# Performance work log

Measured on AMD Instinct MI355X. Metric: run time of the kernel, lower is better.

The kernel has to match this reference:

```python
import jax, jax.numpy as jnp
import numpy as np

D_MODEL = 1024
D_FF = 4096
NUM_EXPERTS = 8
TOP_K = 2
TEMPERATURE = 1.0


def setup_inputs() -> dict:
    key = jax.random.key(0)
    ks = jax.random.split(key, 5)
    hidden_states = jax.random.normal(ks[0], (4, 2048, D_MODEL), dtype=jnp.float32)
    # Router gate: nn.Linear(d_model, num_experts, bias=False), weight [E, d], std=0.01
    gate_w = jax.random.normal(ks[1], (NUM_EXPERTS, D_MODEL), dtype=jnp.float32) * 0.01
    # Expert FFN weights: torch Linear weight is [out, in]; init std=0.02, biases zero
    w1 = jax.random.normal(ks[2], (NUM_EXPERTS, D_FF, D_MODEL), dtype=jnp.float32) * 0.02
    b1 = jnp.zeros((NUM_EXPERTS, D_FF), dtype=jnp.float32)
    w2 = jax.random.normal(ks[3], (NUM_EXPERTS, D_MODEL, D_FF), dtype=jnp.float32) * 0.02
    b2 = jnp.zeros((NUM_EXPERTS, D_MODEL), dtype=jnp.float32)
    return {"hidden_states": hidden_states, "gate_w": gate_w,
            "w1": w1, "b1": b1, "w2": w2, "b2": b2}


def reference(hidden_states, gate_w, w1, b1, w2, b2):
    B, S, D = hidden_states.shape
    E, K = NUM_EXPERTS, TOP_K
    x = hidden_states.reshape(-1, D)  # [T, d]
    T = x.shape[0]

    # --- Router (fp32, eval mode: no noise) ---
    logits = jnp.einsum('td,ed->te', x, gate_w) / TEMPERATURE  # [T, E]
    probs = jax.nn.softmax(logits, axis=-1)
    top_vals, top_idx = jax.lax.top_k(probs, K)               # [T, K]
    weights = top_vals / jnp.sum(top_vals, axis=-1, keepdims=True)

    # Dense combine weights per expert: [T, E]
    one_hot = jax.nn.one_hot(top_idx, E, dtype=x.dtype)        # [T, K, E]
    combine = jnp.einsum('tke,tk->te', one_hot, weights)       # [T, E]

    # --- Load-balancing aux loss ---
    importance = jnp.mean(probs, axis=0)                       # [E]
    load = jnp.sum(one_hot, axis=(0, 1)) / (T * K)             # [E]
    aux_loss = E * jnp.sum(importance * load)

    # --- Expert dispatch/combine (loop over fixed small E) ---
    out = jnp.zeros_like(x)
    for e in range(E):
        h = jax.nn.gelu(x @ w1[e].T + b1[e], approximate=False)  # [T, d_ff]
        y = h @ w2[e].T + b2[e]                                   # [T, d]
        out = out + combine[:, e:e + 1] * y

    return out.reshape(B, S, D), aux_loss
```

## Files before the change

### kernel.cpp

```cpp
#include <hip/hip_runtime.h>
#include <cstdint>
#include <math.h>

#define T_TOK 8192
#define DM 1024
#define DFF 4096
#define NE 8
#define WLMAX 136

typedef __attribute__((ext_vector_type(8))) short short8;
typedef __attribute__((ext_vector_type(4))) float f32x4;

#define GLDS16(g, l) __builtin_amdgcn_global_load_lds( \
    (const __attribute__((address_space(1))) void*)(g), \
    (__attribute__((address_space(3))) void*)(l), 16, 0, 0)

static __device__ __forceinline__ unsigned short f2bf(float f) {
    union { float f; unsigned int u; } v; v.f = f;
    unsigned int r = (v.u + 0x7FFFu + ((v.u >> 16) & 1u)) >> 16;
    return (unsigned short)r;
}

static __device__ __forceinline__ float gelu_f(float v) {
    float z = fabsf(v) * 0.70710678118654752f;
    float t = 1.f / (1.f + 0.3275911f * z);
    float p = t * (0.254829592f + t * (-0.284496736f + t * (1.421413741f +
              t * (-1.453152027f + t * 1.061405429f))));
    float erfz = 1.f - p * __expf(-z * z);
    float s = (v >= 0.f) ? erfz : -erfz;
    return 0.5f * v * (1.f + s);
}

__global__ __launch_bounds__(256) void conv_flat(const float* __restrict__ src,
                                                 unsigned short* __restrict__ dst,
                                                 long long n)
{
    long long i = ((long long)blockIdx.x * 256 + threadIdx.x) * 4;
    if (i >= n) return;
    const float4 v = *(const float4*)(src + i);
    uint2 u;
    u.x = (unsigned)f2bf(v.x) | ((unsigned)f2bf(v.y) << 16);
    u.y = (unsigned)f2bf(v.z) | ((unsigned)f2bf(v.w) << 16);
    *(uint2*)(dst + i) = u;
}

__global__ __launch_bounds__(256) void conv_rows(const float* __restrict__ src,
                                                 unsigned short* __restrict__ dst,
                                                 long long src_off, long long src_stride,
                                                 int ncols)
{
    long long row = blockIdx.y;
    int c = (blockIdx.x * 256 + threadIdx.x) * 4;
    if (c >= ncols) return;
    const float4 v = *(const float4*)(src + src_off + row * src_stride + c);
    uint2 u;
    u.x = (unsigned)f2bf(v.x) | ((unsigned)f2bf(v.y) << 16);
    u.y = (unsigned)f2bf(v.z) | ((unsigned)f2bf(v.w) << 16);
    *(uint2*)(dst + row * (long long)ncols + c) = u;
}

__global__ __launch_bounds__(256) void router_kernel(
    const float* __restrict__ x, const float* __restrict__ gw,
    int* __restrict__ counts, float* __restrict__ imp,
    int* __restrict__ ptok, float* __restrict__ pw)
{
    __shared__ float4 sgw[NE * 256];
    __shared__ float simp[NE];
    const int tid = threadIdx.x;
    #pragma unroll
    for (int j = 0; j < 8; ++j) sgw[tid + j * 256] = ((const float4*)gw)[tid + j * 256];
    if (tid < NE) simp[tid] = 0.f;
    __syncthreads();

    const int wid = tid >> 6, lane = tid & 63;
    const int t = blockIdx.x * 4 + wid;
    float acc[NE];
    #pragma unroll
    for (int e = 0; e < NE; ++e) acc[e] = 0.f;
    const float4* xr = (const float4*)(x + (size_t)t * DM);
    #pragma unroll
    for (int j = 0; j < 4; ++j) {
        int idx = lane + j * 64;
        float4 xv = xr[idx];
        #pragma unroll
        for (int e = 0; e < NE; ++e) {
            float4 g = sgw[e * 256 + idx];
            acc[e] += xv.x * g.x + xv.y * g.y + xv.z * g.z + xv.w * g.w;
        }
    }
    #pragma unroll
    for (int off = 32; off; off >>= 1) {
        #pragma unroll
        for (int e = 0; e < NE; ++e) acc[e] += __shfl_xor(acc[e], off);
    }
    if (lane == 0) {
        float m = acc[0];
        #pragma unroll
        for (int e = 1; e < NE; ++e) m = fmaxf(m, acc[e]);
        float p[NE], s = 0.f;
        #pragma unroll
        for (int e = 0; e < NE; ++e) { p[e] = expf(acc[e] - m); s += p[e]; }
        float inv = 1.f / s;
        #pragma unroll
        for (int e = 0; e < NE; ++e) { p[e] *= inv; atomicAdd(&simp[e], p[e]); }
        int i0 = 0;
        #pragma unroll
        for (int e = 1; e < NE; ++e) if (p[e] > p[i0]) i0 = e;
        int i1 = (i0 == 0) ? 1 : 0;
        #pragma unroll
        for (int e = 0; e < NE; ++e) if (e != i0 && p[e] > p[i1]) i1 = e;
        float v0 = p[i0], v1 = p[i1], wsum = v0 + v1;
        int s0 = atomicAdd(&counts[i0], 1);
        ptok[i0 * T_TOK + s0] = t; pw[i0 * T_TOK + s0] = v0 / wsum;
        int s1 = atomicAdd(&counts[i1], 1);
        ptok[i1 * T_TOK + s1] = t; pw[i1 * T_TOK + s1] = v1 / wsum;
    }
    __syncthreads();
    if (tid < NE) atomicAdd(&imp[tid], simp[tid]);
}

__global__ void finalize_kernel(const int* __restrict__ counts,
                                const float* __restrict__ imp,
                                int* __restrict__ offs, int* __restrict__ wl,
                                float* __restrict__ aux_out)
{
    if (threadIdx.x == 0 && blockIdx.x == 0) {
        int o = 0; float aux = 0.f;
        for (int e = 0; e < NE; ++e) {
            offs[e] = o; o += counts[e];
            aux += (imp[e] / (float)T_TOK) * ((float)counts[e] / (float)(T_TOK * 2));
        }
        offs[NE] = o;
        int it = 0;
        for (int e = 0; e < NE; ++e) {
            int mts = (counts[e] + 127) >> 7;
            for (int mt = 0; mt < mts; ++mt) wl[it++] = (e << 16) | mt;
        }
        for (; it < WLMAX; ++it) wl[it] = -1;
        *aux_out = (float)NE * aux;
    }
}

__global__ __launch_bounds__(256) void pregather_kernel(
    const float* __restrict__ x, const int* __restrict__ counts,
    const int* __restrict__ offs, const int* __restrict__ ptok,
    unsigned short* __restrict__ xg, int* __restrict__ tc, int* __restrict__ tokpair)
{
    const int e = blockIdx.y;
    const int slot = blockIdx.x * 4 + (threadIdx.x >> 6);
    if (slot >= counts[e]) return;
    const int tok = ptok[e * T_TOK + slot];
    const int lane = threadIdx.x & 63;
    const int p = offs[e] + slot;
    if (lane == 0) {
        int k = atomicAdd(&tc[tok], 1);
        tokpair[tok * 2 + k] = p;
    }
    const float4* src = (const float4*)(x + (size_t)tok * DM);
    uint2* dst = (uint2*)(xg + (size_t)p * DM);
    #pragma unroll
    for (int j = 0; j < 4; ++j) {
        float4 v = src[lane + j * 64];
        uint2 u;
        u.x = (unsigned)f2bf(v.x) | ((unsigned)f2bf(v.y) << 16);
        u.y = (unsigned)f2bf(v.z) | ((unsigned)f2bf(v.w) << 16);
        dst[lane + j * 64] = u;
    }
}

__global__ __launch_bounds__(256) void combine_kernel(
    const float* __restrict__ yv, const int* __restrict__ tokpair,
    float* __restrict__ out)
{
    const int t = blockIdx.x;
    const int c = threadIdx.x;
    const long long p0 = tokpair[t * 2], p1 = tokpair[t * 2 + 1];
    const float4 a = ((const float4*)(yv + p0 * DM))[c];
    const float4 b = ((const float4*)(yv + p1 * DM))[c];
    float4 o;
    o.x = a.x + b.x; o.y = a.y + b.y; o.z = a.z + b.z; o.w = a.w + b.w;
    ((float4*)(out + (long long)t * DM))[c] = o;
}

template<int EPI>
__global__ __launch_bounds__(256, 2) void gemm_bt(
    const unsigned short* __restrict__ A,
    const unsigned short* __restrict__ W,
    const float* __restrict__ bias,
    const int* __restrict__ counts, const int* __restrict__ offs,
    const int* __restrict__ ptok, const float* __restrict__ pw,
    const int* __restrict__ wl,
    unsigned short* __restrict__ Hout, float* __restrict__ yv,
    int FFC, int cch, int wfull)
{
    const int bx = blockIdx.x;
    const int item = wl[(bx & 7) * 17 + (bx >> 3)];
    if (item < 0) return;
    const int e = item >> 16, mt = item & 0xffff;
    const int n_e = counts[e];
    int rows_here = n_e - mt * 128; if (rows_here > 128) rows_here = 128;
    const long long row_lo = (long long)offs[e] + (long long)mt * 128;
    const int nt = blockIdx.y;
    const int KD = (EPI == 0) ? DM : FFC;

    __shared__ unsigned short lA[128 * 64];
    __shared__ unsigned short lB[256 * 64];

    const int tid = threadIdx.x, lane = tid & 63, wid = tid >> 6;
    const int nsub = wid * 64;
    const int hi = lane >> 4, lo = lane & 15;

    int wrow0; long long wstride, wcol0;
    if (EPI == 0) {
        wrow0 = e * (wfull ? DFF : FFC) + (wfull ? cch * FFC : 0) + nt * 256;
        wstride = DM; wcol0 = 0;
    } else {
        wrow0 = e * DM + nt * 256;
        wstride = (wfull ? DFF : FFC); wcol0 = (wfull ? (long long)cch * FFC : 0);
    }

    const unsigned short* aaddr[4];
    #pragma unroll
    for (int j = 0; j < 4; ++j) {
        int li = tid + j * 256;
        int r = li >> 3;
        int scol = ((li & 7) ^ (r & 7)) * 8;
        int rc = (r < rows_here) ? r : (rows_here - 1);
        aaddr[j] = A + (row_lo + rc) * KD + scol;
    }
    const unsigned short* baddr[8];
    #pragma unroll
    for (int j = 0; j < 8; ++j) {
        int li = tid + j * 256;
        int r = li >> 3;
        int scol = ((li & 7) ^ (r & 7)) * 8;
        baddr[j] = W + (long long)(wrow0 + r) * wstride + wcol0 + scol;
    }

    f32x4 acc[8][4];
    #pragma unroll
    for (int i = 0; i < 8; ++i)
        #pragma unroll
        for (int j = 0; j < 4; ++j) acc[i][j] = (f32x4)0.f;

    const int NT = KD >> 6;
    for (int t = 0; t < NT; ++t) {
        const long long k0 = (long long)t * 64;
        #pragma unroll
        for (int j = 0; j < 4; ++j) GLDS16(aaddr[j] + k0, &lA[(tid + j * 256) * 8]);
        #pragma unroll
        for (int j = 0; j < 8; ++j) GLDS16(baddr[j] + k0, &lB[(tid + j * 256) * 8]);
        __syncthreads();
        #pragma unroll
        for (int kk = 0; kk < 2; ++kk) {
            short8 af[8], bf[4];
            #pragma unroll
            for (int mi = 0; mi < 8; ++mi) {
                int row = mi * 16 + lo;
                af[mi] = *(const short8*)(&lA[row * 64 + (((kk * 4 + hi) ^ (row & 7)) * 8)]);
            }
            #pragma unroll
            for (int nj = 0; nj < 4; ++nj) {
                int row = nsub + nj * 16 + lo;
                bf[nj] = *(const short8*)(&lB[row * 64 + (((kk * 4 + hi) ^ (row & 7)) * 8)]);
            }
            #pragma unroll
            for (int mi = 0; mi < 8; ++mi)
                #pragma unroll
                for (int nj = 0; nj < 4; ++nj)
                    acc[mi][nj] = __builtin_amdgcn_mfma_f32_16x16x32_bf16(af[mi], bf[nj], acc[mi][nj], 0, 0, 0);
        }
        __syncthreads();
    }

    const int rbase = hi * 4;
    if (EPI == 0) {
        #pragma unroll
        for (int mi = 0; mi < 8; ++mi) {
            #pragma unroll
            for (int r = 0; r < 4; ++r) {
                int m = mi * 16 + rbase + r;
                if (m >= rows_here) continue;
                long long hrow = (row_lo + m) * FFC;
                #pragma unroll
                for (int nj = 0; nj < 4; ++nj) {
                    int f = nt * 256 + nsub + nj * 16 + lo;
                    float v = acc[mi][nj][r] + bias[e * DFF + cch * FFC + f];
                    Hout[hrow + f] = f2bf(gelu_f(v));
                }
            }
        }
    } else {
        #pragma unroll
        for (int mi = 0; mi < 8; ++mi) {
            #pragma unroll
            for (int r = 0; r < 4; ++r) {
                int m = mi * 16 + rbase + r;
                if (m >= rows_here) continue;
                int pidx = e * T_TOK + mt * 128 + m;
                float wgt = pw[pidx];
                float* yrow = yv + (row_lo + m) * DM;
                #pragma unroll
                for (int nj = 0; nj < 4; ++nj) {
                    int d = nt * 256 + nsub + nj * 16 + lo;
                    float v = acc[mi][nj][r];
                    if (cch == 0) yrow[d] = wgt * (v + bias[e * DM + d]);
                    else          yrow[d] += wgt * v;
                }
            }
        }
    }
}

extern "C" void kernel_launch(void* const* d_in, const int* in_sizes, int n_in,
                              void* d_out, int out_size, void* d_ws, size_t ws_size,
                              hipStream_t stream)
{
    const float* x  = (const float*)d_in[0];
    const float* gw = (const float*)d_in[1];
    const float* w1 = (const float*)d_in[2];
    const float* b1 = (const float*)d_in[3];
    const float* w2 = (const float*)d_in[4];
    const float* b2 = (const float*)d_in[5];
    float* out = (float*)d_out;

    char* ws = (char*)d_ws;
    int*   counts  = (int*)ws;
    float* imp     = (float*)(ws + 64);
    int*   offs    = (int*)(ws + 128);
    int*   tc      = (int*)(ws + 256);
    int*   wl      = (int*)(ws + 33024);
    int*   tokpair = (int*)(ws + 33792);
    int*   ptok    = (int*)(ws + 99840);
    float* pw      = (float*)(ws + 99840 + (size_t)NE * T_TOK * 4);
    size_t cur = 99840 + (size_t)NE * T_TOK * 8;
    cur = (cur + 511) & ~(size_t)511;

    unsigned short* xg = (unsigned short*)(ws + cur);
    cur += (size_t)2 * T_TOK * DM * 2;
    cur = (cur + 511) & ~(size_t)511;
    float* yv = (float*)(ws + cur);
    cur += (size_t)2 * T_TOK * DM * 4;

    const size_t wfull_bytes = (size_t)NE * DFF * DM * 2;
    const size_t hrow_total  = 2 * (size_t)T_TOK;

    int FFC = 0, wfull = 0;
    unsigned short *w1b = nullptr, *w2b = nullptr, *H = nullptr;
    for (int f = DFF; f >= 256; f >>= 1) {
        size_t need = cur + 2 * wfull_bytes + hrow_total * (size_t)f * 2;
        if (need <= ws_size) { FFC = f; wfull = 1; break; }
    }
    if (wfull) {
        w1b = (unsigned short*)(ws + cur); cur += wfull_bytes;
        w2b = (unsigned short*)(ws + cur); cur += wfull_bytes;
        H   = (unsigned short*)(ws + cur);
    } else {
        for (int f = 2048; f >= 256; f >>= 1) {
            size_t wc = (size_t)NE * f * DM * 2;
            size_t need = cur + 2 * wc + hrow_total * (size_t)f * 2;
            if (need <= ws_size) { FFC = f; break; }
        }
        if (FFC == 0) return;
        size_t wc = (size_t)NE * FFC * DM * 2;
        w1b = (unsigned short*)(ws + cur); cur += wc;
        w2b = (unsigned short*)(ws + cur); cur += wc;
        H   = (unsigned short*)(ws + cur);
    }

    hipMemsetAsync(ws, 0, 33024, stream);

    router_kernel<<<T_TOK / 4, 256, 0, stream>>>(x, gw, counts, imp, ptok, pw);
    finalize_kernel<<<1, 64, 0, stream>>>(counts, imp, offs, wl, out + (size_t)out_size - 1);
    {
        dim3 gp(T_TOK / 4, NE);
        pregather_kernel<<<gp, 256, 0, stream>>>(x, counts, offs, ptok, xg, tc, tokpair);
    }
    if (wfull) {
        long long n = (long long)NE * DFF * DM;
        conv_flat<<<(unsigned)(n / 1024), 256, 0, stream>>>(w1, w1b, n);
        conv_flat<<<(unsigned)(n / 1024), 256, 0, stream>>>(w2, w2b, n);
    }

    const int NCH = DFF / FFC;
    for (int c = 0; c < NCH; ++c) {
        if (!wfull) {
            dim3 gc1((unsigned)((long long)FFC * DM / 1024), NE);
            conv_rows<<<gc1, 256, 0, stream>>>(w1, w1b,
                (long long)c * FFC * DM, (long long)DFF * DM, FFC * DM);
            dim3 gc2((unsigned)((FFC + 1023) / 1024), NE * DM);
            conv_rows<<<gc2, 256, 0, stream>>>(w2, w2b,
                (long long)c * FFC, (long long)DFF, FFC);
        }
        dim3 g1(WLMAX, FFC / 256, 1);
        gemm_bt<0><<<g1, 256, 0, stream>>>(xg, w1b, b1, counts, offs, ptok, pw, wl, H, yv, FFC, c, wfull);
        dim3 g2(WLMAX, DM / 256, 1);
        gemm_bt<1><<<g2, 256, 0, stream>>>(H, w2b, b2, counts, offs, ptok, pw, wl, H, yv, FFC, c, wfull);
    }
    combine_kernel<<<T_TOK, 256, 0, stream>>>(yv, tokpair, out);
}
```

Before: 814.2 us.

## Replace LDS-staged GEMM with direct global-to-register MFMA loads on 128x128 tiles

Removes the shared-memory staging (global_load_lds plus barriers) from the expert GEMM and has each wave load its MFMA fragments straight from global memory, double-buffering them in registers. The block tile shrinks from 128x256 to 128x128 with a 2x2 wave layout, which doubles the grid along N. This drops LDS traffic and barriers but gives up intra-block operand reuse, so global/L2 traffic per MFMA rises and the fragment loads are strided 16-byte accesses.

```diff
diff --git a/kernel.cpp b/kernel.cpp
--- a/kernel.cpp
+++ b/kernel.cpp
@@ -10,10 +10,6 @@
 
 typedef __attribute__((ext_vector_type(8))) short short8;
 typedef __attribute__((ext_vector_type(4))) float f32x4;
-
-#define GLDS16(g, l) __builtin_amdgcn_global_load_lds( \
-    (const __attribute__((address_space(1))) void*)(g), \
-    (__attribute__((address_space(3))) void*)(l), 16, 0, 0)
 
 static __device__ __forceinline__ unsigned short f2bf(float f) {
     union { float f; unsigned int u; } v; v.f = f;
@@ -203,88 +199,79 @@
     const int nt = blockIdx.y;
     const int KD = (EPI == 0) ? DM : FFC;
 
-    __shared__ unsigned short lA[128 * 64];
-    __shared__ unsigned short lB[256 * 64];
-
     const int tid = threadIdx.x, lane = tid & 63, wid = tid >> 6;
-    const int nsub = wid * 64;
+    const int msub = (wid & 1) * 64, nsub = (wid >> 1) * 64;
     const int hi = lane >> 4, lo = lane & 15;
 
     int wrow0; long long wstride, wcol0;
     if (EPI == 0) {
-        wrow0 = e * (wfull ? DFF : FFC) + (wfull ? cch * FFC : 0) + nt * 256;
+        wrow0 = e * (wfull ? DFF : FFC) + (wfull ? cch * FFC : 0) + nt * 128;
         wstride = DM; wcol0 = 0;
     } else {
-        wrow0 = e * DM + nt * 256;
+        wrow0 = e * DM + nt * 128;
         wstride = (wfull ? DFF : FFC); wcol0 = (wfull ? (long long)cch * FFC : 0);
     }
 
-    const unsigned short* aaddr[4];
-    #pragma unroll
-    for (int j = 0; j < 4; ++j) {
-        int li = tid + j * 256;
-        int r = li >> 3;
-        int scol = ((li & 7) ^ (r & 7)) * 8;
-        int rc = (r < rows_here) ? r : (rows_here - 1);
-        aaddr[j] = A + (row_lo + rc) * KD + scol;
-    }
-    const unsigned short* baddr[8];
-    #pragma unroll
-    for (int j = 0; j < 8; ++j) {
-        int li = tid + j * 256;
-        int r = li >> 3;
-        int scol = ((li & 7) ^ (r & 7)) * 8;
-        baddr[j] = W + (long long)(wrow0 + r) * wstride + wcol0 + scol;
-    }
-
-    f32x4 acc[8][4];
-    #pragma unroll
-    for (int i = 0; i < 8; ++i)
+    const unsigned short* ap[4];
+    const unsigned short* bp[4];
+    #pragma unroll
+    for (int i = 0; i < 4; ++i) {
+        int ar = msub + i * 16 + lo;
+        int arc = (ar < rows_here) ? ar : (rows_here - 1);
+        ap[i] = A + (row_lo + arc) * KD + hi * 8;
+        bp[i] = W + (long long)(wrow0 + nsub + i * 16 + lo) * wstride + wcol0 + hi * 8;
+    }
+
+    f32x4 acc[4][4];
+    #pragma unroll
+    for (int i = 0; i < 4; ++i)
         #pragma unroll
         for (int j = 0; j < 4; ++j) acc[i][j] = (f32x4)0.f;
 
-    const int NT = KD >> 6;
-    for (int t = 0; t < NT; ++t) {
-        const long long k0 = (long long)t * 64;
-        #pragma unroll
-        for (int j = 0; j < 4; ++j) GLDS16(aaddr[j] + k0, &lA[(tid + j * 256) * 8]);
-        #pragma unroll
-        for (int j = 0; j < 8; ++j) GLDS16(baddr[j] + k0, &lB[(tid + j * 256) * 8]);
-        __syncthreads();
-        #pragma unroll
-        for (int kk = 0; kk < 2; ++kk) {
-            short8 af[8], bf[4];
-            #pragma unroll
-            for (int mi = 0; mi < 8; ++mi) {
-                int row = mi * 16 + lo;
-                af[mi] = *(const short8*)(&lA[row * 64 + (((kk * 4 + hi) ^ (row & 7)) * 8)]);
+    const int S = KD >> 5;
+    short8 a0[4], b0[4], a1[4], b1[4];
+    #pragma unroll
+    for (int i = 0; i < 4; ++i) { a0[i] = *(const short8*)(ap[i]); b0[i] = *(const short8*)(bp[i]); }
+
+    for (int s = 0; s < S; s += 2) {
+        const long long o1 = (long long)(s + 1) * 32;
+        #pragma unroll
+        for (int i = 0; i < 4; ++i) {
+            a1[i] = *(const short8*)(ap[i] + o1);
+            b1[i] = *(const short8*)(bp[i] + o1);
+        }
+        #pragma unroll
+        for (int mi = 0; mi < 4; ++mi)
+            #pragma unroll
+            for (int nj = 0; nj < 4; ++nj)
+                acc[mi][nj] = __builtin_amdgcn_mfma_f32_16x16x32_bf16(a0[mi], b0[nj], acc[mi][nj], 0, 0, 0);
+        if (s + 2 < S) {
+            const long long o2 = (long long)(s + 2) * 32;
+            #pragma unroll
+            for (int i = 0; i < 4; ++i) {
+                a0[i] = *(const short8*)(ap[i] + o2);
+                b0[i] = *(const short8*)(bp[i] + o2);
             }
-            #pragma unroll
-            for (int nj = 0; nj < 4; ++nj) {
-                int row = nsub + nj * 16 + lo;
-                bf[nj] = *(const short8*)(&lB[row * 64 + (((kk * 4 + hi) ^ (row & 7)) * 8)]);
-            }
-            #pragma unroll
-            for (int mi = 0; mi < 8; ++mi)
-                #pragma unroll
-                for (int nj = 0; nj < 4; ++nj)
-                    acc[mi][nj] = __builtin_amdgcn_mfma_f32_16x16x32_bf16(af[mi], bf[nj], acc[mi][nj], 0, 0, 0);
-        }
-        __syncthreads();
+        }
+        #pragma unroll
+        for (int mi = 0; mi < 4; ++mi)
+            #pragma unroll
+            for (int nj = 0; nj < 4; ++nj)
+                acc[mi][nj] = __builtin_amdgcn_mfma_f32_16x16x32_bf16(a1[mi], b1[nj], acc[mi][nj], 0, 0, 0);
     }
 
     const int rbase = hi * 4;
     if (EPI == 0) {
         #pragma unroll
-        for (int mi = 0; mi < 8; ++mi) {
+        for (int mi = 0; mi < 4; ++mi) {
             #pragma unroll
             for (int r = 0; r < 4; ++r) {
-                int m = mi * 16 + rbase + r;
-                if (m >= rows_here) continue;
-                long long hrow = (row_lo + m) * FFC;
+                int mloc = msub + mi * 16 + rbase + r;
+                if (mloc >= rows_here) continue;
+                long long hrow = (row_lo + mloc) * FFC;
                 #pragma unroll
                 for (int nj = 0; nj < 4; ++nj) {
-                    int f = nt * 256 + nsub + nj * 16 + lo;
+                    int f = nt * 128 + nsub + nj * 16 + lo;
                     float v = acc[mi][nj][r] + bias[e * DFF + cch * FFC + f];
                     Hout[hrow + f] = f2bf(gelu_f(v));
                 }
@@ -292,17 +279,17 @@
         }
     } else {
         #pragma unroll
-        for (int mi = 0; mi < 8; ++mi) {
+        for (int mi = 0; mi < 4; ++mi) {
             #pragma unroll
             for (int r = 0; r < 4; ++r) {
-                int m = mi * 16 + rbase + r;
-                if (m >= rows_here) continue;
-                int pidx = e * T_TOK + mt * 128 + m;
+                int mloc = msub + mi * 16 + rbase + r;
+                if (mloc >= rows_here) continue;
+                int pidx = e * T_TOK + mt * 128 + mloc;
                 float wgt = pw[pidx];
-                float* yrow = yv + (row_lo + m) * DM;
+                float* yrow = yv + (row_lo + mloc) * DM;
                 #pragma unroll
                 for (int nj = 0; nj < 4; ++nj) {
-                    int d = nt * 256 + nsub + nj * 16 + lo;
+                    int d = nt * 128 + nsub + nj * 16 + lo;
                     float v = acc[mi][nj][r];
                     if (cch == 0) yrow[d] = wgt * (v + bias[e * DM + d]);
                     else          yrow[d] += wgt * v;
@@ -392,9 +379,9 @@
             conv_rows<<<gc2, 256, 0, stream>>>(w2, w2b,
                 (long long)c * FFC, (long long)DFF, FFC);
         }
-        dim3 g1(WLMAX, FFC / 256, 1);
+        dim3 g1(WLMAX, FFC / 128, 1);
         gemm_bt<0><<<g1, 256, 0, stream>>>(xg, w1b, b1, counts, offs, ptok, pw, wl, H, yv, FFC, c, wfull);
-        dim3 g2(WLMAX, DM / 256, 1);
+        dim3 g2(WLMAX, DM / 128, 1);
         gemm_bt<1><<<g2, 256, 0, stream>>>(H, w2b, b2, counts, offs, ptok, pw, wl, H, yv, FFC, c, wfull);
     }
     combine_kernel<<<T_TOK, 256, 0, stream>>>(yv, tokpair, out);
```

New measurement: 1.409 ms. 73.1% more time.

## Double-buffer LDS tiles with BK=32 to overlap global loads with MFMA

Applied to the files above, without the earlier changes.

Splits the LDS tiles into two buffers with a K-step of 32 instead of one buffer with 64, and issues the next tile's global-to-LDS loads before computing on the current one. This hides global load latency behind MFMA work and removes one barrier per iteration. The LDS swizzle is changed to suit 32-wide rows, and fragment offsets are precomputed. The cost is twice as many loop iterations, each with less work per barrier. The single sync per iteration relies on the asynchronous LDS loads having completed by that barrier.

```diff
diff --git a/kernel.cpp b/kernel.cpp
--- a/kernel.cpp
+++ b/kernel.cpp
@@ -203,8 +203,8 @@
     const int nt = blockIdx.y;
     const int KD = (EPI == 0) ? DM : FFC;
 
-    __shared__ unsigned short lA[128 * 64];
-    __shared__ unsigned short lB[256 * 64];
+    __shared__ unsigned short lA[2][128 * 32];
+    __shared__ unsigned short lB[2][256 * 32];
 
     const int tid = threadIdx.x, lane = tid & 63, wid = tid >> 6;
     const int nsub = wid * 64;
@@ -219,22 +219,34 @@
         wstride = (wfull ? DFF : FFC); wcol0 = (wfull ? (long long)cch * FFC : 0);
     }
 
-    const unsigned short* aaddr[4];
+    const unsigned short* aaddr[2];
+    #pragma unroll
+    for (int j = 0; j < 2; ++j) {
+        int li = tid + j * 256;
+        int r = li >> 2;
+        int sg = ((li & 3) ^ ((r >> 1) & 3)) * 8;
+        int rc = (r < rows_here) ? r : (rows_here - 1);
+        aaddr[j] = A + (row_lo + rc) * KD + sg;
+    }
+    const unsigned short* baddr[4];
     #pragma unroll
     for (int j = 0; j < 4; ++j) {
         int li = tid + j * 256;
-        int r = li >> 3;
-        int scol = ((li & 7) ^ (r & 7)) * 8;
-        int rc = (r < rows_here) ? r : (rows_here - 1);
-        aaddr[j] = A + (row_lo + rc) * KD + scol;
-    }
-    const unsigned short* baddr[8];
-    #pragma unroll
-    for (int j = 0; j < 8; ++j) {
-        int li = tid + j * 256;
-        int r = li >> 3;
-        int scol = ((li & 7) ^ (r & 7)) * 8;
-        baddr[j] = W + (long long)(wrow0 + r) * wstride + wcol0 + scol;
+        int r = li >> 2;
+        int sg = ((li & 3) ^ ((r >> 1) & 3)) * 8;
+        baddr[j] = W + (long long)(wrow0 + r) * wstride + wcol0 + sg;
+    }
+
+    int offA[8], offB[4];
+    #pragma unroll
+    for (int mi = 0; mi < 8; ++mi) {
+        int row = mi * 16 + lo;
+        offA[mi] = row * 32 + ((hi ^ ((row >> 1) & 3)) * 8);
+    }
+    #pragma unroll
+    for (int nj = 0; nj < 4; ++nj) {
+        int row = nsub + nj * 16 + lo;
+        offB[nj] = row * 32 + ((hi ^ ((row >> 1) & 3)) * 8);
     }
 
     f32x4 acc[8][4];
@@ -243,34 +255,34 @@
         #pragma unroll
         for (int j = 0; j < 4; ++j) acc[i][j] = (f32x4)0.f;
 
-    const int NT = KD >> 6;
+#define STAGE(buf, t) do { \
+        const long long _k0 = (long long)(t) * 32; \
+        GLDS16(aaddr[0] + _k0, &lA[buf][tid * 8]); \
+        GLDS16(aaddr[1] + _k0, &lA[buf][(tid + 256) * 8]); \
+        _Pragma("unroll") \
+        for (int _j = 0; _j < 4; ++_j) \
+            GLDS16(baddr[_j] + _k0, &lB[buf][(tid + _j * 256) * 8]); \
+    } while (0)
+
+    const int NT = KD >> 5;
+    STAGE(0, 0);
+    __syncthreads();
+
+    int cur = 0;
     for (int t = 0; t < NT; ++t) {
-        const long long k0 = (long long)t * 64;
-        #pragma unroll
-        for (int j = 0; j < 4; ++j) GLDS16(aaddr[j] + k0, &lA[(tid + j * 256) * 8]);
-        #pragma unroll
-        for (int j = 0; j < 8; ++j) GLDS16(baddr[j] + k0, &lB[(tid + j * 256) * 8]);
+        if (t + 1 < NT) STAGE(cur ^ 1, t + 1);
+        short8 af[8], bf[4];
+        #pragma unroll
+        for (int mi = 0; mi < 8; ++mi) af[mi] = *(const short8*)(&lA[cur][offA[mi]]);
+        #pragma unroll
+        for (int nj = 0; nj < 4; ++nj) bf[nj] = *(const short8*)(&lB[cur][offB[nj]]);
+        #pragma unroll
+        for (int mi = 0; mi < 8; ++mi)
+            #pragma unroll
+            for (int nj = 0; nj < 4; ++nj)
+                acc[mi][nj] = __builtin_amdgcn_mfma_f32_16x16x32_bf16(af[mi], bf[nj], acc[mi][nj], 0, 0, 0);
         __syncthreads();
-        #pragma unroll
-        for (int kk = 0; kk < 2; ++kk) {
-            short8 af[8], bf[4];
-            #pragma unroll
-            for (int mi = 0; mi < 8; ++mi) {
-                int row = mi * 16 + lo;
-                af[mi] = *(const short8*)(&lA[row * 64 + (((kk * 4 + hi) ^ (row & 7)) * 8)]);
-            }
-            #pragma unroll
-            for (int nj = 0; nj < 4; ++nj) {
-                int row = nsub + nj * 16 + lo;
-                bf[nj] = *(const short8*)(&lB[row * 64 + (((kk * 4 + hi) ^ (row & 7)) * 8)]);
-            }
-            #pragma unroll
-            for (int mi = 0; mi < 8; ++mi)
-                #pragma unroll
-                for (int nj = 0; nj < 4; ++nj)
-                    acc[mi][nj] = __builtin_amdgcn_mfma_f32_16x16x32_bf16(af[mi], bf[nj], acc[mi][nj], 0, 0, 0);
-        }
-        __syncthreads();
+        cur ^= 1;
     }
 
     const int rbase = hi * 4;
@@ -310,6 +322,7 @@
             }
         }
     }
+#undef STAGE
 }
 
 extern "C" void kernel_launch(void* const* d_in, const int* in_sizes, int n_in,
```

New measurement: 902.3 us. 10.8% more time.
